# Optimization experiments

Hardware: AMD Instinct MI355X
Metric: run time of the kernel (lower is better)

## Reference

```python
import jax, jax.numpy as jnp
import numpy as np

B, T, C = 2, 2048, 1024
NH, NKV, HD, NG = 16, 8, 64, 8   # heads, kv heads, head_dim, global heads
NG_KV = NG * NKV // NH           # global kv heads = 4
VE_CH = 32                       # ve_gate input channels
WIN = 1024                       # local sliding-window (left) size


def setup_inputs() -> dict:
    key = jax.random.key(0)
    ks = jax.random.split(key, 8)
    x = jax.random.normal(ks[0], (B, T, C), jnp.float32)
    ve = jax.random.normal(ks[1], (B, T, NKV * HD), jnp.float32)
    # true rotary tables over half the head dim
    half = HD // 2
    inv_freq = 1.0 / (10000.0 ** (np.arange(half, dtype=np.float64) / half))
    ang = np.arange(T, dtype=np.float64)[:, None] * inv_freq[None, :]
    cos = jnp.asarray(np.cos(ang), jnp.float32)[None, :, None, :]  # [1,T,1,32]
    sin = jnp.asarray(np.sin(ang), jnp.float32)[None, :, None, :]
    s = C ** -0.5
    Wq = jax.random.normal(ks[2], (C, NH * HD), jnp.float32) * s
    Wk = jax.random.normal(ks[3], (C, NKV * HD), jnp.float32) * s
    Wv = jax.random.normal(ks[4], (C, NKV * HD), jnp.float32) * s
    Wproj = jax.random.normal(ks[5], (C, C), jnp.float32) * s
    Wg = jax.random.normal(ks[6], (VE_CH, NKV), jnp.float32) * (VE_CH ** -0.5)
    return dict(x=x, ve=ve, cos=cos, sin=sin, Wq=Wq, Wk=Wk, Wv=Wv,
                Wproj=Wproj, Wg=Wg, window=WIN)


def _rope(x, cos, sin):
    d = x.shape[-1] // 2
    x1, x2 = x[..., :d], x[..., d:]
    return jnp.concatenate([x1 * cos + x2 * sin, -x1 * sin + x2 * cos], axis=-1)


def _rms_norm(x):
    eps = jnp.asarray(jnp.finfo(x.dtype).eps, x.dtype)
    return x * jax.lax.rsqrt(jnp.mean(x * x, axis=-1, keepdims=True) + eps)


def _gqa_attn(q, k, v, left_window):
    # q: [B,T,Hq,D]; k,v: [B,T,Hk,D]; GQA with g = Hq//Hk queries per kv head.
    b, t, hq, d = q.shape
    hk = k.shape[2]
    g = hq // hk
    qg = q.reshape(b, t, hk, g, d)
    scores = jnp.einsum('bqhgd,bkhd->bhgqk', qg, k) * (d ** -0.5)
    i = jnp.arange(t)[:, None]
    j = jnp.arange(t)[None, :]
    if left_window < 0:
        mask = j <= i                       # full causal
    else:
        mask = (j <= i) & ((i - j) <= left_window)  # causal sliding window
    scores = jnp.where(mask, scores, jnp.asarray(-1e30, scores.dtype))
    p = jax.nn.softmax(scores, axis=-1)
    out = jnp.einsum('bhgqk,bkhd->bqhgd', p, v)
    return out.reshape(b, t, hq, d)


def reference(x, ve, cos, sin, Wq, Wk, Wv, Wproj, Wg, window):
    b, t, c = x.shape
    q = (x @ Wq).reshape(b, t, NH, HD)
    k = (x @ Wk).reshape(b, t, NKV, HD)
    v = (x @ Wv).reshape(b, t, NKV, HD)
    # value-embedding gating: gate = 2*sigmoid(Linear(x[..., :32])) per kv head
    gate = 2.0 * jax.nn.sigmoid(x[..., :VE_CH] @ Wg)       # [B,T,NKV]
    v = v + gate[..., None] * ve.reshape(b, t, NKV, HD)
    # inline RoPE then RMSNorm on q and k
    q = _rms_norm(_rope(q, cos, sin))
    k = _rms_norm(_rope(k, cos, sin))
    # split global (full causal) vs local (windowed) head groups
    y_global = _gqa_attn(q[:, :, :NG], k[:, :, :NG_KV], v[:, :, :NG_KV], -1)
    y_local = _gqa_attn(q[:, :, NG:], k[:, :, NG_KV:], v[:, :, NG_KV:], window)
    y = jnp.concatenate([y_global, y_local], axis=2).reshape(b, t, c)
    return y @ Wproj
```

## Files before the change

kernel.cpp:

```cpp
#include <hip/hip_runtime.h>
#include <hip/hip_bf16.h>
#include <math.h>

typedef __bf16 bf16x8 __attribute__((ext_vector_type(8)));
typedef __bf16 bf16x4 __attribute__((ext_vector_type(4)));
typedef float  f32x4  __attribute__((ext_vector_type(4)));

#define MFMA16(a, b, c) __builtin_amdgcn_mfma_f32_16x16x32_bf16((a), (b), (c), 0, 0, 0)

__device__ __forceinline__ void gload16(const void* g, void* lds) {
    __builtin_amdgcn_global_load_lds(
        (const __attribute__((address_space(1))) uint32_t*)g,
        (__attribute__((address_space(3))) uint32_t*)lds, 16, 0, 0);
}

__global__ __launch_bounds__(256)
void prep2_kernel(const float* __restrict__ x, __bf16* __restrict__ xb,
                  const float* __restrict__ Wq, const float* __restrict__ Wk,
                  const float* __restrict__ Wv, const float* __restrict__ Wproj,
                  __bf16* __restrict__ wqkvt, __bf16* __restrict__ wprojt) {
    const int bx = blockIdx.x;
    const int tid = threadIdx.x;
    if (bx < 4096) {
        int i = bx * 256 + tid;
        float4 v = reinterpret_cast<const float4*>(x)[i];
        bf16x4 o = { (__bf16)v.x, (__bf16)v.y, (__bf16)v.z, (__bf16)v.w };
        *reinterpret_cast<bf16x4*>(xb + (size_t)i * 4) = o;
        return;
    }
    __shared__ __bf16 Ts[64 * 72];
    const int idx = bx - 4096;
    const int z = idx >> 8;
    const float* W = (z == 0) ? Wq : (z == 1) ? Wk : (z == 2) ? Wv : Wproj;
    __bf16* dst = (z == 3) ? wprojt : wqkvt;
    const int N = (z == 1 || z == 2) ? 512 : 1024;
    const int nt_off = (z == 1) ? 1024 : (z == 2) ? 1536 : 0;
    const int n0 = (idx & 15) * 64, k0 = ((idx >> 4) & 15) * 64;
    if (n0 >= N) return;
    {
        int r = tid >> 2;
        int c0 = (tid & 3) * 16;
        const float4* s4 = reinterpret_cast<const float4*>(
            W + (size_t)(k0 + r) * N + n0 + c0);
        float val[16];
        #pragma unroll
        for (int q = 0; q < 4; ++q) {
            float4 v = s4[q];
            val[q * 4 + 0] = v.x; val[q * 4 + 1] = v.y;
            val[q * 4 + 2] = v.z; val[q * 4 + 3] = v.w;
        }
        #pragma unroll
        for (int j = 0; j < 16; ++j) Ts[(c0 + j) * 72 + r] = (__bf16)val[j];
    }
    __syncthreads();
    {
        int n = tid >> 2, kg = (tid & 3) * 16;
        __bf16* out = dst + (size_t)(nt_off + n0 + n) * 1024 + k0 + kg;
        bf16x8 t0 = *reinterpret_cast<const bf16x8*>(&Ts[n * 72 + kg]);
        bf16x8 t1 = *reinterpret_cast<const bf16x8*>(&Ts[n * 72 + kg + 8]);
        *reinterpret_cast<bf16x8*>(out) = t0;
        *reinterpret_cast<bf16x8*>(out + 8) = t1;
    }
}

template <typename OutT>
__global__ __launch_bounds__(256)
void gemm_bf16(const __bf16* __restrict__ A, const __bf16* __restrict__ Bt,
               OutT* __restrict__ C, int M, int N, int K) {
    __shared__ __align__(16) __bf16 As[128 * 64];
    __shared__ __align__(16) __bf16 Bs[128 * 64];
    const int tid = threadIdx.x;
    const int lane = tid & 63, w = tid >> 6;
    const int wr = w >> 1, wc = w & 1;
    const int nwg = gridDim.x * gridDim.y;
    const int id = blockIdx.y * gridDim.x + blockIdx.x;
    const int nid = (id & 7) * (nwg >> 3) + (id >> 3);
    const int bxs = nid % gridDim.x, bys = nid / gridDim.x;
    const int bm = bys * 128, bn = bxs * 128;
    const int lhi = lane >> 4, llo = lane & 15;
    const int gsrc = (lane & 7) ^ ((lane >> 3) & 7);

    f32x4 acc[4][4] = {};

    for (int k0 = 0; k0 < K; k0 += 64) {
        __syncthreads();
        const __bf16* Ab = A + (size_t)bm * K + k0;
        const __bf16* Bb = Bt + (size_t)bn * K + k0;
        #pragma unroll
        for (int rr = 0; rr < 4; ++rr) {
            int c = rr * 4 + w;
            int r = c * 8 + (lane >> 3);
            gload16(Ab + (size_t)r * K + gsrc * 8, (char*)As + c * 1024);
            gload16(Bb + (size_t)r * K + gsrc * 8, (char*)Bs + c * 1024);
        }
        __syncthreads();

        #pragma unroll
        for (int ks = 0; ks < 2; ++ks) {
            bf16x8 af[4], bfr[4];
            int g = ks * 4 + lhi;
            #pragma unroll
            for (int i = 0; i < 4; ++i) {
                int ra = wr * 64 + i * 16 + llo;
                af[i] = *reinterpret_cast<const bf16x8*>(
                    (const char*)As + ra * 128 + ((g ^ (ra & 7)) << 4));
                int rb = wc * 64 + i * 16 + llo;
                bfr[i] = *reinterpret_cast<const bf16x8*>(
                    (const char*)Bs + rb * 128 + ((g ^ (rb & 7)) << 4));
            }
            #pragma unroll
            for (int i = 0; i < 4; ++i)
                #pragma unroll
                for (int j = 0; j < 4; ++j)
                    acc[i][j] = MFMA16(af[i], bfr[j], acc[i][j]);
        }
    }

    #pragma unroll
    for (int i = 0; i < 4; ++i) {
        #pragma unroll
        for (int j = 0; j < 4; ++j) {
            int col = bn + wc * 64 + j * 16 + llo;
            #pragma unroll
            for (int r = 0; r < 4; ++r) {
                int row = bm + wr * 64 + i * 16 + lhi * 4 + r;
                C[(size_t)row * N + col] = (OutT)acc[i][j][r];
            }
        }
    }
}

__global__ __launch_bounds__(256)
void post_kernel(__bf16* __restrict__ qkv, const float* __restrict__ x,
                 const float* __restrict__ ve, const float* __restrict__ Wg,
                 const float* __restrict__ cosb, const float* __restrict__ sinb,
                 __bf16* __restrict__ vT) {
    const int id = blockIdx.x;
    const int tid = threadIdx.x;
    if (id < 24576) {
        const int u = id >> 10;
        const int row = (id & 1023) * 4 + (tid >> 6);
        const int d = tid & 63;
        const int t = row & 2047;
        const int off = (u < 16) ? u * 64 : 1024 + (u - 16) * 64;
        __bf16* p = qkv + (size_t)row * 2048 + off;
        float v = (float)p[d];
        float partner = __shfl(v, d ^ 32, 64);
        float r;
        if (d < 32) {
            float cs = cosb[t * 32 + d], sn = sinb[t * 32 + d];
            r = v * cs + partner * sn;
        } else {
            float cs = cosb[t * 32 + d - 32], sn = sinb[t * 32 + d - 32];
            r = -partner * sn + v * cs;
        }
        float s = r * r;
        #pragma unroll
        for (int mm = 1; mm < 64; mm <<= 1) s += __shfl_xor(s, mm, 64);
        r *= rsqrtf(s * (1.0f / 64.0f) + 1.1920929e-07f);
        if (u < 16) r *= 0.18033688011116012f;
        p[d] = (__bf16)r;
    } else {
        __shared__ __bf16 Ts[64 * 72];
        const int rem = id - 24576;
        const int ch = rem & 63;
        const int h = rem >> 6;
        {
            int r = tid >> 2, c0 = (tid & 3) * 16;
            int grow = ch * 64 + r;
            float gz = 0.f;
            {
                const float* xr = x + (size_t)grow * 1024 + (tid & 3) * 8;
                #pragma unroll
                for (int i = 0; i < 8; ++i)
                    gz = fmaf(xr[i], Wg[((tid & 3) * 8 + i) * 8 + h], gz);
                gz += __shfl_xor(gz, 1, 64);
                gz += __shfl_xor(gz, 2, 64);
            }
            float g = 2.0f / (1.0f + expf(-gz));
            const __bf16* vp = qkv + (size_t)grow * 2048 + 1536 + h * 64 + c0;
            const float* vep = ve + (size_t)grow * 512 + h * 64 + c0;
            bf16x8 v0 = *reinterpret_cast<const bf16x8*>(vp);
            bf16x8 v1 = *reinterpret_cast<const bf16x8*>(vp + 8);
            #pragma unroll
            for (int j = 0; j < 8; ++j) {
                Ts[(c0 + j) * 72 + r]     = (__bf16)((float)v0[j] + g * vep[j]);
                Ts[(c0 + 8 + j) * 72 + r] = (__bf16)((float)v1[j] + g * vep[8 + j]);
            }
        }
        __syncthreads();
        {
            int d = tid >> 2, t0l = (tid & 3) * 16;
            int b = ch >> 5, tloc = (ch & 31) * 64;
            __bf16* out = vT + ((size_t)((b * 8 + h) * 64 + d)) * 2048 + tloc + t0l;
            bf16x8 t0 = *reinterpret_cast<const bf16x8*>(&Ts[d * 72 + t0l]);
            bf16x8 t1 = *reinterpret_cast<const bf16x8*>(&Ts[d * 72 + t0l + 8]);
            *reinterpret_cast<bf16x8*>(out) = t0;
            *reinterpret_cast<bf16x8*>(out + 8) = t1;
        }
    }
}

__global__ __launch_bounds__(256, 4)
void attn_mfma(const __bf16* __restrict__ qkv, const __bf16* __restrict__ vT,
               __bf16* __restrict__ y, const int* __restrict__ winp) {
    __shared__ __align__(16) __bf16 Ks[2][64 * 64];
    __shared__ __align__(16) __bf16 VTs[2][64 * 64];
    __shared__ __align__(16) __bf16 Ps[4][16 * 64];

    const int bid = blockIdx.x;
    const int kvh = bid & 7;
    int tdec = bid >> 3;
    const int b = tdec & 1; tdec >>= 1;
    const int qh = tdec & 1;
    const int qt = 31 - (tdec >> 1);
    const int h = (kvh < 4) ? (kvh * 2 + qh) : (8 + (kvh - 4) * 2 + qh);
    const int q0 = qt * 64;
    const int tid = threadIdx.x, lane = tid & 63, w = tid >> 6;
    const int lhi = lane >> 4, llo = lane & 15;
    const int gsrc = (lane & 7) ^ ((lane >> 3) & 7);
    const int win = (h < 8) ? -1 : winp[0];
    const int winv = (win < 0) ? (1 << 30) : win;

    const __bf16* kbase = qkv + (size_t)(b * 2048) * 2048 + 1024 + kvh * 64;
    const __bf16* vtbase = vT + ((size_t)((b * 8 + kvh) * 64)) * 2048;

    int kts = 0;
    if (win >= 0) { int s = q0 - win; if (s > 0) kts = s >> 6; }

    const __bf16* qrow = qkv + (size_t)(b * 2048 + q0 + w * 16 + llo) * 2048
                         + h * 64 + lhi * 8;
    bf16x8 qf[2];
    qf[0] = *(const bf16x8*)(qrow);
    qf[1] = *(const bf16x8*)(qrow + 32);

    auto STAGE = [&](int buf, int ktx) {
        #pragma unroll
        for (int rr = 0; rr < 2; ++rr) {
            int c = rr * 4 + w;
            int r = c * 8 + (lane >> 3);
            gload16(kbase + (size_t)(ktx * 64 + r) * 2048 + gsrc * 8,
                    (char*)&Ks[buf][0] + c * 1024);
            gload16(vtbase + (size_t)r * 2048 + ktx * 64 + gsrc * 8,
                    (char*)&VTs[buf][0] + c * 1024);
        }
    };

    f32x4 oaccT[4] = {};
    float lrow = 0.f;
    int cur = 0;
    STAGE(0, kts);

    const int pswz = (llo & 7) << 4;

    for (int kt = kts; kt <= qt; ++kt) {
        __syncthreads();
        if (kt < qt) STAGE(cur ^ 1, kt + 1);

        f32x4 sacc[4] = {};
        __builtin_amdgcn_s_setprio(1);
        #pragma unroll
        for (int ks = 0; ks < 2; ++ks) {
            #pragma unroll
            for (int kj = 0; kj < 4; ++kj) {
                int rb = kj * 16 + llo;
                bf16x8 bk = *(const bf16x8*)((const char*)&Ks[cur][0]
                    + rb * 128 + (((ks * 4 + lhi) ^ (rb & 7)) << 4));
                sacc[kj] = MFMA16(bk, qf[ks], sacc[kj]);
            }
        }
        __builtin_amdgcn_s_setprio(0);

        const bool needMask = (kt == qt) || (win >= 0 && kt * 64 < q0 + 63 - winv);

        float sv[16];
        #pragma unroll
        for (int kj = 0; kj < 4; ++kj)
            #pragma unroll
            for (int r = 0; r < 4; ++r)
                sv[kj * 4 + r] = sacc[kj][r];
        if (needMask) {
            int qrowi = q0 + w * 16 + llo;
            #pragma unroll
            for (int kj = 0; kj < 4; ++kj)
                #pragma unroll
                for (int r = 0; r < 4; ++r) {
                    int key = kt * 64 + kj * 16 + lhi * 4 + r;
                    bool ok = (key <= qrowi) && (qrowi - key <= winv);
                    if (!ok) sv[kj * 4 + r] = -__builtin_inff();
                }
        }

        float p[16], rs = 0.f;
        #pragma unroll
        for (int t = 0; t < 16; ++t) {
            p[t] = __builtin_amdgcn_exp2f(sv[t] - 12.0f);
            rs += p[t];
        }
        lrow += rs;

        #pragma unroll
        for (int kj = 0; kj < 4; ++kj) {
            bf16x4 pk = { (__bf16)p[kj * 4 + 0], (__bf16)p[kj * 4 + 1],
                          (__bf16)p[kj * 4 + 2], (__bf16)p[kj * 4 + 3] };
            *(bf16x4*)((char*)&Ps[w][0]
                + ((llo * 128 + kj * 32 + lhi * 8) ^ pswz)) = pk;
        }

        __builtin_amdgcn_s_setprio(1);
        #pragma unroll
        for (int ks = 0; ks < 2; ++ks) {
            bf16x8 ap = *(const bf16x8*)((const char*)&Ps[w][0]
                + ((llo * 128 + ks * 64 + lhi * 16) ^ pswz));
            #pragma unroll
            for (int dj = 0; dj < 4; ++dj) {
                int rv = dj * 16 + llo;
                bf16x8 bv = *(const bf16x8*)((const char*)&VTs[cur][0]
                    + rv * 128 + (((ks * 4 + lhi) ^ (rv & 7)) << 4));
                oaccT[dj] = MFMA16(bv, ap, oaccT[dj]);
            }
        }
        __builtin_amdgcn_s_setprio(0);
        cur ^= 1;
    }

    lrow += __shfl_xor(lrow, 16, 64);
    lrow += __shfl_xor(lrow, 32, 64);

    float inv = 1.0f / lrow;
    int row = b * 2048 + q0 + w * 16 + llo;
    #pragma unroll
    for (int dj = 0; dj < 4; ++dj) {
        bf16x4 o = { (__bf16)(oaccT[dj][0] * inv), (__bf16)(oaccT[dj][1] * inv),
                     (__bf16)(oaccT[dj][2] * inv), (__bf16)(oaccT[dj][3] * inv) };
        *(bf16x4*)(&y[(size_t)row * 1024 + h * 64 + dj * 16 + lhi * 4]) = o;
    }
}

extern "C" void kernel_launch(void* const* d_in, const int* in_sizes, int n_in,
                              void* d_out, int out_size, void* d_ws, size_t ws_size,
                              hipStream_t stream) {
    const float* x     = (const float*)d_in[0];
    const float* ve    = (const float*)d_in[1];
    const float* cosb  = (const float*)d_in[2];
    const float* sinb  = (const float*)d_in[3];
    const float* Wq    = (const float*)d_in[4];
    const float* Wk    = (const float*)d_in[5];
    const float* Wv    = (const float*)d_in[6];
    const float* Wproj = (const float*)d_in[7];
    const float* Wg    = (const float*)d_in[8];
    const int*   winp  = (const int*)d_in[9];

    char* ws = (char*)d_ws;
    __bf16* qkv    = (__bf16*)(ws);
    __bf16* vT     = (__bf16*)(ws + (16u << 20));
    __bf16* ybuf   = (__bf16*)(ws + (20u << 20));
    __bf16* xb     = (__bf16*)(ws + (28u << 20));
    __bf16* wqkvt  = (__bf16*)(ws + (36u << 20));
    __bf16* wprojt = (__bf16*)(ws + (40u << 20));

    prep2_kernel<<<5120, 256, 0, stream>>>(x, xb, Wq, Wk, Wv, Wproj, wqkvt, wprojt);
    gemm_bf16<__bf16><<<dim3(16, 32), 256, 0, stream>>>(xb, wqkvt, qkv, 4096, 2048, 1024);
    post_kernel<<<25088, 256, 0, stream>>>(qkv, x, ve, Wg, cosb, sinb, vT);
    attn_mfma<<<1024, 256, 0, stream>>>(qkv, vT, ybuf, winp);
    gemm_bf16<float><<<dim3(8, 32), 256, 0, stream>>>(ybuf, wprojt, (float*)d_out, 4096, 1024, 1024);
}
```

Before: 118.1 us.

## Replace double-buffered LDS DMA staging with register prefetch into single LDS buffer

The attention kernel stops double-buffering K and V^T tiles in LDS through direct global-to-LDS loads. It now prefetches the next tile into registers during compute, then writes it to a single swizzled LDS buffer between two barriers. This halves the K/V LDS footprint, which could allow more resident blocks, but it adds a second barrier per iteration and VGPR pressure. The fixed -12 exponent offset is dropped and the per-row probability sum becomes a tree reduction done after the P write.

```diff
diff --git a/kernel.cpp b/kernel.cpp
--- a/kernel.cpp
+++ b/kernel.cpp
@@ -204,8 +204,8 @@
 __global__ __launch_bounds__(256, 4)
 void attn_mfma(const __bf16* __restrict__ qkv, const __bf16* __restrict__ vT,
                __bf16* __restrict__ y, const int* __restrict__ winp) {
-    __shared__ __align__(16) __bf16 Ks[2][64 * 64];
-    __shared__ __align__(16) __bf16 VTs[2][64 * 64];
+    __shared__ __align__(16) __bf16 Ks[64 * 64];
+    __shared__ __align__(16) __bf16 VTs[64 * 64];
     __shared__ __align__(16) __bf16 Ps[4][16 * 64];
 
     const int bid = blockIdx.x;
@@ -218,7 +218,6 @@
     const int q0 = qt * 64;
     const int tid = threadIdx.x, lane = tid & 63, w = tid >> 6;
     const int lhi = lane >> 4, llo = lane & 15;
-    const int gsrc = (lane & 7) ^ ((lane >> 3) & 7);
     const int win = (h < 8) ? -1 : winp[0];
     const int winv = (win < 0) ? (1 << 30) : win;
 
@@ -234,28 +233,37 @@
     qf[0] = *(const bf16x8*)(qrow);
     qf[1] = *(const bf16x8*)(qrow + 32);
 
-    auto STAGE = [&](int buf, int ktx) {
+    uint4 kreg[2], vreg[2];
+    auto LOADR = [&](int ktx) {
         #pragma unroll
         for (int rr = 0; rr < 2; ++rr) {
-            int c = rr * 4 + w;
-            int r = c * 8 + (lane >> 3);
-            gload16(kbase + (size_t)(ktx * 64 + r) * 2048 + gsrc * 8,
-                    (char*)&Ks[buf][0] + c * 1024);
-            gload16(vtbase + (size_t)r * 2048 + ktx * 64 + gsrc * 8,
-                    (char*)&VTs[buf][0] + c * 1024);
+            int rk = (rr * 4 + w) * 8 + (lane >> 3);
+            int co = (lane & 7) * 8;
+            kreg[rr] = *(const uint4*)(kbase + (size_t)(ktx * 64 + rk) * 2048 + co);
+            vreg[rr] = *(const uint4*)(vtbase + (size_t)rk * 2048 + ktx * 64 + co);
+        }
+    };
+    auto WRITES = [&]() {
+        #pragma unroll
+        for (int rr = 0; rr < 2; ++rr) {
+            int rk = (rr * 4 + w) * 8 + (lane >> 3);
+            int off = rk * 128 + (((lane & 7) ^ (rk & 7)) << 4);
+            *(uint4*)((char*)Ks + off) = kreg[rr];
+            *(uint4*)((char*)VTs + off) = vreg[rr];
         }
     };
 
     f32x4 oaccT[4] = {};
     float lrow = 0.f;
-    int cur = 0;
-    STAGE(0, kts);
+
+    LOADR(kts);
+    WRITES();
+    __syncthreads();
 
     const int pswz = (llo & 7) << 4;
 
     for (int kt = kts; kt <= qt; ++kt) {
-        __syncthreads();
-        if (kt < qt) STAGE(cur ^ 1, kt + 1);
+        if (kt < qt) LOADR(kt + 1);
 
         f32x4 sacc[4] = {};
         __builtin_amdgcn_s_setprio(1);
@@ -264,7 +272,7 @@
             #pragma unroll
             for (int kj = 0; kj < 4; ++kj) {
                 int rb = kj * 16 + llo;
-                bf16x8 bk = *(const bf16x8*)((const char*)&Ks[cur][0]
+                bf16x8 bk = *(const bf16x8*)((const char*)&Ks[0]
                     + rb * 128 + (((ks * 4 + lhi) ^ (rb & 7)) << 4));
                 sacc[kj] = MFMA16(bk, qf[ks], sacc[kj]);
             }
@@ -291,13 +299,10 @@
                 }
         }
 
-        float p[16], rs = 0.f;
-        #pragma unroll
-        for (int t = 0; t < 16; ++t) {
-            p[t] = __builtin_amdgcn_exp2f(sv[t] - 12.0f);
-            rs += p[t];
-        }
-        lrow += rs;
+        float p[16];
+        #pragma unroll
+        for (int t = 0; t < 16; ++t)
+            p[t] = __builtin_amdgcn_exp2f(sv[t]);
 
         #pragma unroll
         for (int kj = 0; kj < 4; ++kj) {
@@ -307,6 +312,12 @@
                 + ((llo * 128 + kj * 32 + lhi * 8) ^ pswz)) = pk;
         }
 
+        #pragma unroll
+        for (int st = 8; st >= 1; st >>= 1)
+            #pragma unroll
+            for (int t = 0; t < st; ++t) p[t] += p[t + st];
+        lrow += p[0];
+
         __builtin_amdgcn_s_setprio(1);
         #pragma unroll
         for (int ks = 0; ks < 2; ++ks) {
@@ -315,13 +326,18 @@
             #pragma unroll
             for (int dj = 0; dj < 4; ++dj) {
                 int rv = dj * 16 + llo;
-                bf16x8 bv = *(const bf16x8*)((const char*)&VTs[cur][0]
+                bf16x8 bv = *(const bf16x8*)((const char*)&VTs[0]
                     + rv * 128 + (((ks * 4 + lhi) ^ (rv & 7)) << 4));
                 oaccT[dj] = MFMA16(bv, ap, oaccT[dj]);
             }
         }
         __builtin_amdgcn_s_setprio(0);
-        cur ^= 1;
+
+        if (kt < qt) {
+            __syncthreads();
+            WRITES();
+            __syncthreads();
+        }
     }
 
     lrow += __shfl_xor(lrow, 16, 64);
```

Measured after the change: 168.3 us. +42.5%, slower.
